# Kernel tuning notes

Hardware: AMD Instinct MI355X
Metric: run time of the kernel (lower is better)

Reference implementation:

```python
import jax, jax.numpy as jnp
import numpy as np

IN_DIM, OUT_DIM, N_PROTO, RANK = 1024, 1024, 32, 16


def setup_inputs() -> dict:
    key = jax.random.key(0)
    ks = jax.random.split(key, 5)
    x = jax.random.normal(ks[0], (2, 4096, IN_DIM), dtype=jnp.float32)
    prototypes = jax.random.normal(ks[1], (N_PROTO, IN_DIM), dtype=jnp.float32) * 0.02
    B = jax.random.normal(ks[2], (N_PROTO, RANK, IN_DIM), dtype=jnp.float32) * 0.02
    A = jax.random.normal(ks[3], (N_PROTO, OUT_DIM, RANK), dtype=jnp.float32) * 0.02
    bias = jnp.zeros((N_PROTO, OUT_DIM), dtype=jnp.float32)
    temp = jnp.asarray(1.0, dtype=jnp.float32)
    return {"x": x, "prototypes": prototypes, "B": B, "A": A, "bias": bias, "temp": temp}


def reference(x, prototypes, B, A, bias, temp):
    lead = x.shape[:-1]
    xf = x.reshape(-1, IN_DIM)                       # [N, in]
    x2 = jnp.sum(xf * xf, axis=1, keepdims=True)     # [N,1]
    p2 = jnp.sum(prototypes * prototypes, axis=1)    # [P]
    d2 = x2 + p2[None, :] - 2.0 * (xf @ prototypes.T)
    dists = jnp.sqrt(jnp.maximum(d2, 0.0))           # [N,P]
    t = jnp.maximum(jnp.abs(temp), 0.1)
    w = jax.nn.softmax(-dists / t, axis=1)           # [N,P]
    topw, topi = jax.lax.top_k(w, 2)                 # [N,2]
    topw = topw / jnp.sum(topw, axis=1, keepdims=True)
    out = jnp.zeros((xf.shape[0], OUT_DIM), dtype=xf.dtype)
    for tslot in range(2):
        idx = topi[:, tslot]                          # [N]
        wt = topw[:, tslot:tslot + 1]                 # [N,1]
        h = jnp.einsum('nri,ni->nr', B[idx], xf)      # gathered low-rank down-proj
        y = jnp.einsum('nor,nr->no', A[idx], h) + bias[idx]
        out = out + wt * y
    return out.reshape(*lead, OUT_DIM)
```

## Files before the change

kernel.cpp:

```cpp
#include <hip/hip_runtime.h>
#include <math.h>

#define ROWS_TOTAL 8192
#define KDIM 1024
#define NPROTO 32
#define RNK 16
#define OUTD 1024
#define TIE_EPS 1.30e-4

__global__ __launch_bounds__(256) void route_kernel(
    const float* __restrict__ x, const float* __restrict__ proto,
    const float* __restrict__ temp, float4* __restrict__ route,
    int* __restrict__ counts)
{
    __shared__ float Xs[16][68];
    __shared__ float Ps[64][33];
    __shared__ double x2s[16];
    __shared__ double p2s[32];
    __shared__ int lcnt[64];

    const int tid = threadIdx.x;
    const int rowbase = blockIdx.x * 16;
    const int frow = tid >> 4;
    const int fq   = tid & 15;
    const int c    = tid & 31;
    const int rg   = tid >> 5;

    if (tid < 64) lcnt[tid] = 0;

    double xsq = 0.0, p2a = 0.0, p2b = 0.0;
    double acc0 = 0.0, acc1 = 0.0;

    for (int kc = 0; kc < KDIM; kc += 64) {
        float4 xv = *(const float4*)(x + (rowbase + frow) * KDIM + kc + 4 * fq);
        xsq = fma((double)xv.x, (double)xv.x, xsq);
        xsq = fma((double)xv.y, (double)xv.y, xsq);
        xsq = fma((double)xv.z, (double)xv.z, xsq);
        xsq = fma((double)xv.w, (double)xv.w, xsq);
        *(float4*)(&Xs[frow][4 * fq]) = xv;
        float4 pa = *(const float4*)(proto + frow * KDIM + kc + 4 * fq);
        float4 pb = *(const float4*)(proto + (frow + 16) * KDIM + kc + 4 * fq);
        p2a = fma((double)pa.x, (double)pa.x, p2a);
        p2a = fma((double)pa.y, (double)pa.y, p2a);
        p2a = fma((double)pa.z, (double)pa.z, p2a);
        p2a = fma((double)pa.w, (double)pa.w, p2a);
        p2b = fma((double)pb.x, (double)pb.x, p2b);
        p2b = fma((double)pb.y, (double)pb.y, p2b);
        p2b = fma((double)pb.z, (double)pb.z, p2b);
        p2b = fma((double)pb.w, (double)pb.w, p2b);
        Ps[4 * fq + 0][frow] = pa.x;
        Ps[4 * fq + 1][frow] = pa.y;
        Ps[4 * fq + 2][frow] = pa.z;
        Ps[4 * fq + 3][frow] = pa.w;
        Ps[4 * fq + 0][frow + 16] = pb.x;
        Ps[4 * fq + 1][frow + 16] = pb.y;
        Ps[4 * fq + 2][frow + 16] = pb.z;
        Ps[4 * fq + 3][frow + 16] = pb.w;
        __syncthreads();
        #pragma unroll
        for (int k = 0; k < 64; k += 4) {
            float4 xa = *(const float4*)(&Xs[2 * rg][k]);
            float4 xb = *(const float4*)(&Xs[2 * rg + 1][k]);
            double q0 = (double)Ps[k][c],     q1 = (double)Ps[k + 1][c];
            double q2 = (double)Ps[k + 2][c], q3 = (double)Ps[k + 3][c];
            acc0 = fma((double)xa.x, q0, acc0);
            acc0 = fma((double)xa.y, q1, acc0);
            acc0 = fma((double)xa.z, q2, acc0);
            acc0 = fma((double)xa.w, q3, acc0);
            acc1 = fma((double)xb.x, q0, acc1);
            acc1 = fma((double)xb.y, q1, acc1);
            acc1 = fma((double)xb.z, q2, acc1);
            acc1 = fma((double)xb.w, q3, acc1);
        }
        __syncthreads();
    }

    #pragma unroll
    for (int m = 1; m < 16; m <<= 1) {
        xsq += __shfl_xor(xsq, m);
        p2a += __shfl_xor(p2a, m);
        p2b += __shfl_xor(p2b, m);
    }
    if (fq == 0) { x2s[frow] = xsq; p2s[frow] = p2a; p2s[frow + 16] = p2b; }
    __syncthreads();

    const double tmp = (double)fmaxf(fabsf(temp[0]), 0.1f);
    const double myp2 = p2s[c];

    #pragma unroll
    for (int which = 0; which < 2; ++which) {
        double key = myp2 - 2.0 * (which ? acc1 : acc0);
        double k1 = key, k2 = 1.0e300, k3 = 1.1e300;
        int    i1 = c,   i2 = 64,      i3 = 65;
        #pragma unroll
        for (int m = 1; m < 32; m <<= 1) {
            double b1 = __shfl_xor(k1, m), b2 = __shfl_xor(k2, m), b3 = __shfl_xor(k3, m);
            int    j1 = __shfl_xor(i1, m), j2 = __shfl_xor(i2, m), j3 = __shfl_xor(i3, m);
            bool c1 = k1 <= b1;
            double m1 = c1 ? k1 : b1, M1 = c1 ? b1 : k1;
            int   mi1 = c1 ? i1 : j1, Mi1 = c1 ? j1 : i1;
            bool c2 = k2 <= b2;
            double m2 = c2 ? k2 : b2;
            int   mi2 = c2 ? i2 : j2;
            bool c3 = k3 <= b3;
            double m3 = c3 ? k3 : b3;
            int   mi3 = c3 ? i3 : j3;
            bool c4 = M1 <= m2;
            double t2 = c4 ? M1 : m2,  T2 = c4 ? m2 : M1;
            int   ti2 = c4 ? Mi1 : mi2, Ti2 = c4 ? mi2 : Mi1;
            bool c5 = T2 <= m3;
            k1 = m1; i1 = mi1;
            k2 = t2; i2 = ti2;
            k3 = c5 ? T2 : m3; i3 = c5 ? Ti2 : mi3;
        }
        if (c == 0) {
            const int row = rowbase + 2 * rg + which;
            bool tie = (k3 - k2) < TIE_EPS;
            bool take3 = tie && (i3 < i2);
            double ksel = take3 ? k3 : k2;
            int    isel = take3 ? i3 : i2;
            double x2 = x2s[2 * rg + which];
            double d0 = sqrt(fmax(x2 + k1, 0.0));
            double d1 = sqrt(fmax(x2 + ksel, 0.0));
            float e  = expf((float)((d0 - d1) / tmp));
            float w0 = 1.f / (1.f + e);
            route[row] = make_float4(__int_as_float(i1), __int_as_float(isel),
                                     w0, e * w0);
            atomicAdd(&lcnt[i1], 1);
            atomicAdd(&lcnt[32 + isel], 1);
        }
    }
    __syncthreads();
    if (tid < 64) atomicAdd(&counts[tid], lcnt[tid]);
}

__global__ __launch_bounds__(64) void scan_kernel(int* __restrict__ counts,
                                                  int2* __restrict__ segs)
{
    const int tid = threadIdx.x;
    int v = counts[tid];
    int sum = v;
    #pragma unroll
    for (int off = 1; off < 32; off <<= 1) {
        int u = __shfl_up(sum, off, 32);
        if ((tid & 31) >= off) sum += u;
    }
    int excl = sum - v;
    counts[tid] = excl;
    segs[tid] = make_int2(excl, excl + v);
}

__global__ __launch_bounds__(256) void scatter_kernel(
    const float4* __restrict__ route, int* __restrict__ counts,
    int* __restrict__ rowlist0, int* __restrict__ rowlist1)
{
    __shared__ int lcnt[64];
    __shared__ int gbase[64];
    const int tid = threadIdx.x;
    const int i = blockIdx.x * 256 + tid;
    if (tid < 64) lcnt[tid] = 0;
    __syncthreads();
    float4 rt = route[i];
    int p0 = __float_as_int(rt.x);
    int p1 = __float_as_int(rt.y);
    int lp0 = atomicAdd(&lcnt[p0], 1);
    int lp1 = atomicAdd(&lcnt[32 + p1], 1);
    __syncthreads();
    if (tid < 64) gbase[tid] = atomicAdd(&counts[tid], lcnt[tid]);
    __syncthreads();
    rowlist0[gbase[p0] + lp0] = i;
    rowlist1[gbase[32 + p1] + lp1] = i;
}

__global__ __launch_bounds__(256) void transpose_kernel(
    const float* __restrict__ A, const float* __restrict__ B,
    float* __restrict__ At, float* __restrict__ Bt)
{
    __shared__ float T[16 * 68];
    __shared__ float U[64 * 20];
    const int tid = threadIdx.x;
    const int p = blockIdx.x;
    const float4* B4 = (const float4*)(B + (size_t)p * RNK * KDIM);
    const float4* A4 = (const float4*)(A + (size_t)p * OUTD * RNK);
    float4* Bt4 = (float4*)(Bt + (size_t)p * KDIM * RNK);
    float4* At4 = (float4*)(At + (size_t)p * RNK * OUTD);

    for (int c = 0; c < 16; ++c) {
        {
            int r = tid >> 4, kk = tid & 15;
            float4 v = B4[r * 256 + c * 16 + kk];
            *(float4*)&T[r * 68 + kk * 4] = v;
        }
        {
            int o = tid >> 2, rq = tid & 3;
            float4 v = A4[(c * 64 + o) * 4 + rq];
            *(float4*)&U[o * 20 + rq * 4] = v;
        }
        __syncthreads();
        {
            int k = tid >> 2, rq = tid & 3;
            float4 g = make_float4(T[(rq * 4 + 0) * 68 + k], T[(rq * 4 + 1) * 68 + k],
                                   T[(rq * 4 + 2) * 68 + k], T[(rq * 4 + 3) * 68 + k]);
            Bt4[(c * 64 + k) * 4 + rq] = g;
        }
        {
            int r = tid >> 4, ow = tid & 15;
            float4 g = make_float4(U[(ow * 4 + 0) * 20 + r], U[(ow * 4 + 1) * 20 + r],
                                   U[(ow * 4 + 2) * 20 + r], U[(ow * 4 + 3) * 20 + r]);
            At4[r * 256 + c * 16 + ow] = g;
        }
        __syncthreads();
    }
}

__global__ __launch_bounds__(256) void h_kernel(
    const float* __restrict__ x, const float* __restrict__ Bt,
    const int* __restrict__ rowlist0, const int* __restrict__ rowlist1,
    const int2* __restrict__ segs, float* __restrict__ hws)
{
    __shared__ float part[4][4][17];
    __shared__ int xoffs[4];

    const int tid = threadIdx.x;
    const int w = tid >> 6, l = tid & 63;
    const int kq = l >> 2, rq = l & 3;
    const int s = blockIdx.y;
    const int slot = s >> 5;
    const int2 sg = segs[s];
    const int* rl = slot ? rowlist1 : rowlist0;
    const float4* Btp = (const float4*)(Bt + (size_t)(s & 31) * KDIM * RNK);
    const int qbase = w * 256;

    for (int c = blockIdx.x; ; c += gridDim.x) {
        const int base = sg.x + c * 4;
        if (base >= sg.y) break;
        const int m = min(4, sg.y - base);

        if (tid < 4) xoffs[tid] = rl[base + min(tid, m - 1)] * KDIM;
        __syncthreads();
        const int x0 = xoffs[0], x1 = xoffs[1], x2 = xoffs[2], x3 = xoffs[3];

        float4 a0 = {0,0,0,0}, a1 = {0,0,0,0}, a2 = {0,0,0,0}, a3 = {0,0,0,0};
        #pragma unroll
        for (int i = 0; i < 16; ++i) {
            const int k = qbase + i * 16 + kq;
            float4 bv = Btp[k * 4 + rq];
            float v0 = x[x0 + k], v1 = x[x1 + k], v2 = x[x2 + k], v3 = x[x3 + k];
            a0.x = fmaf(v0, bv.x, a0.x); a0.y = fmaf(v0, bv.y, a0.y);
            a0.z = fmaf(v0, bv.z, a0.z); a0.w = fmaf(v0, bv.w, a0.w);
            a1.x = fmaf(v1, bv.x, a1.x); a1.y = fmaf(v1, bv.y, a1.y);
            a1.z = fmaf(v1, bv.z, a1.z); a1.w = fmaf(v1, bv.w, a1.w);
            a2.x = fmaf(v2, bv.x, a2.x); a2.y = fmaf(v2, bv.y, a2.y);
            a2.z = fmaf(v2, bv.z, a2.z); a2.w = fmaf(v2, bv.w, a2.w);
            a3.x = fmaf(v3, bv.x, a3.x); a3.y = fmaf(v3, bv.y, a3.y);
            a3.z = fmaf(v3, bv.z, a3.z); a3.w = fmaf(v3, bv.w, a3.w);
        }
        #pragma unroll
        for (int msk = 4; msk < 64; msk <<= 1) {
            a0.x += __shfl_xor(a0.x, msk); a0.y += __shfl_xor(a0.y, msk);
            a0.z += __shfl_xor(a0.z, msk); a0.w += __shfl_xor(a0.w, msk);
            a1.x += __shfl_xor(a1.x, msk); a1.y += __shfl_xor(a1.y, msk);
            a1.z += __shfl_xor(a1.z, msk); a1.w += __shfl_xor(a1.w, msk);
            a2.x += __shfl_xor(a2.x, msk); a2.y += __shfl_xor(a2.y, msk);
            a2.z += __shfl_xor(a2.z, msk); a2.w += __shfl_xor(a2.w, msk);
            a3.x += __shfl_xor(a3.x, msk); a3.y += __shfl_xor(a3.y, msk);
            a3.z += __shfl_xor(a3.z, msk); a3.w += __shfl_xor(a3.w, msk);
        }
        if (kq == 0) {
            *(float4*)&part[w][0][rq * 4] = a0;
            *(float4*)&part[w][1][rq * 4] = a1;
            *(float4*)&part[w][2][rq * 4] = a2;
            *(float4*)&part[w][3][rq * 4] = a3;
        }
        __syncthreads();
        if (tid < 64) {
            const int e = tid >> 4, r = tid & 15;
            if (e < m) {
                float hsum = part[0][e][r] + part[1][e][r]
                           + part[2][e][r] + part[3][e][r];
                hws[(size_t)(slot * ROWS_TOTAL + base + e) * 16 + r] = hsum;
            }
        }
        __syncthreads();
    }
}

__global__ __launch_bounds__(64) void y_kernel(
    const float* __restrict__ At, const float* __restrict__ bias,
    const float4* __restrict__ route, const int* __restrict__ rowlist,
    const int2* __restrict__ segs, const float* __restrict__ hws,
    float* __restrict__ out, int slot)
{
    __shared__ float hsm[4][16];
    __shared__ int rows[4];
    __shared__ float wts[4];

    const int l = threadIdx.x;
    const int p = blockIdx.y;
    const int2 sg = segs[slot * 32 + p];
    const float4* Atp = (const float4*)(At + (size_t)p * RNK * OUTD);
    const float4* bp  = (const float4*)(bias + (size_t)p * OUTD);

    for (int c = blockIdx.x; ; c += gridDim.x) {
        const int base = sg.x + c * 4;
        if (base >= sg.y) break;
        const int m = min(4, sg.y - base);
        const int gbase = slot * ROWS_TOTAL + base;

        if (l < 4) {
            int rr = rowlist[base + min(l, m - 1)];
            rows[l] = rr;
            float4 rt = route[rr];
            wts[l] = slot ? rt.w : rt.z;
        }
        {
            const int e = l >> 4, r = l & 15;
            hsm[e][r] = hws[(size_t)(gbase + min(e, m - 1)) * 16 + r];
        }
        __syncthreads();

        #pragma unroll
        for (int j = 0; j < 4; ++j) {
            const int f4 = j * 64 + l;
            float4 bb = bp[f4];
            float4 c0 = bb, c1 = bb, c2 = bb, c3 = bb;
            #pragma unroll
            for (int r = 0; r < 16; ++r) {
                float4 a = Atp[r * 256 + f4];
                float h0 = hsm[0][r], h1 = hsm[1][r], h2 = hsm[2][r], h3 = hsm[3][r];
                c0.x = fmaf(h0, a.x, c0.x); c0.y = fmaf(h0, a.y, c0.y);
                c0.z = fmaf(h0, a.z, c0.z); c0.w = fmaf(h0, a.w, c0.w);
                c1.x = fmaf(h1, a.x, c1.x); c1.y = fmaf(h1, a.y, c1.y);
                c1.z = fmaf(h1, a.z, c1.z); c1.w = fmaf(h1, a.w, c1.w);
                c2.x = fmaf(h2, a.x, c2.x); c2.y = fmaf(h2, a.y, c2.y);
                c2.z = fmaf(h2, a.z, c2.z); c2.w = fmaf(h2, a.w, c2.w);
                c3.x = fmaf(h3, a.x, c3.x); c3.y = fmaf(h3, a.y, c3.y);
                c3.z = fmaf(h3, a.z, c3.z); c3.w = fmaf(h3, a.w, c3.w);
            }
            #pragma unroll
            for (int e = 0; e < 4; ++e) {
                if (e < m) {
                    float4 cc = (e == 0) ? c0 : (e == 1) ? c1 : (e == 2) ? c2 : c3;
                    const float w = wts[e];
                    float4 v = make_float4(w * cc.x, w * cc.y, w * cc.z, w * cc.w);
                    float4* dst = (float4*)(out + (size_t)rows[e] * OUTD + f4 * 4);
                    if (slot) {
                        float4 old = *dst;
                        v.x += old.x; v.y += old.y; v.z += old.z; v.w += old.w;
                    }
                    *dst = v;
                }
            }
        }
        __syncthreads();
    }
}

extern "C" void kernel_launch(void* const* d_in, const int* in_sizes, int n_in,
                              void* d_out, int out_size, void* d_ws, size_t ws_size,
                              hipStream_t stream) {
    const float* x     = (const float*)d_in[0];
    const float* proto = (const float*)d_in[1];
    const float* B     = (const float*)d_in[2];
    const float* A     = (const float*)d_in[3];
    const float* bias  = (const float*)d_in[4];
    const float* temp  = (const float*)d_in[5];
    float* out = (float*)d_out;

    char* wsb = (char*)d_ws;
    float4* route = (float4*)wsb;
    int* rowlist0 = (int*)(wsb + 131072);
    int* rowlist1 = rowlist0 + ROWS_TOTAL;
    int* counts   = rowlist1 + ROWS_TOTAL;
    int2* segs    = (int2*)(counts + 64);
    float* Bt     = (float*)(wsb + 262144);
    float* At     = (float*)(wsb + 262144 + 2097152);
    float* hws    = (float*)(wsb + 262144 + 2 * 2097152);

    hipMemsetAsync(counts, 0, 64 * sizeof(int), stream);
    transpose_kernel<<<NPROTO, 256, 0, stream>>>(A, B, At, Bt);
    route_kernel<<<ROWS_TOTAL / 16, 256, 0, stream>>>(x, proto, temp, route, counts);
    scan_kernel<<<1, 64, 0, stream>>>(counts, segs);
    scatter_kernel<<<ROWS_TOTAL / 256, 256, 0, stream>>>(route, counts, rowlist0, rowlist1);
    h_kernel<<<dim3(64, 64), 256, 0, stream>>>(x, Bt, rowlist0, rowlist1, segs, hws);
    y_kernel<<<dim3(64, NPROTO), 64, 0, stream>>>(At, bias, route, rowlist0, segs, hws, out, 0);
    y_kernel<<<dim3(64, NPROTO), 64, 0, stream>>>(At, bias, route, rowlist1, segs, hws, out, 1);
}
```

Before: 175.4 us.

## Restructure routing distance kernel with 4x4 register tiles and split-K reduction

The routing kernel now processes 8 rows per block instead of 16 and stages x and prototypes in shared memory as doubles. Each thread computes a 4x4 register tile over a K slice, followed by shuffle and shared-memory reductions across K lanes and warps. Prototype squared norms move into a separate one-block kernel, so blocks no longer recompute them, and the row norm is accumulated in fp32. This aims to cut per-FMA shared loads and conversions and to double the block count, at the cost of more shared memory, an extra launch, and slightly different rounding of x² near ties.

```diff
diff --git a/kernel.cpp b/kernel.cpp
--- a/kernel.cpp
+++ b/kernel.cpp
@@ -8,127 +8,171 @@
 #define OUTD 1024
 #define TIE_EPS 1.30e-4
 
+__global__ __launch_bounds__(256) void p2_kernel(
+    const float* __restrict__ proto, double* __restrict__ p2g)
+{
+    __shared__ double red[32][9];
+    const int t = threadIdx.x;
+    const int p = t >> 3, seg = t & 7;
+    const float* a = proto + (size_t)p * KDIM + seg * 128;
+    double s = 0.0;
+    for (int k = 0; k < 128; ++k) {
+        double v = (double)a[k];
+        s = fma(v, v, s);
+    }
+    red[p][seg] = s;
+    __syncthreads();
+    if (t < 32) {
+        double acc = red[t][0];
+        #pragma unroll
+        for (int j = 1; j < 8; ++j) acc += red[t][j];
+        p2g[t] = acc;
+    }
+}
+
 __global__ __launch_bounds__(256) void route_kernel(
     const float* __restrict__ x, const float* __restrict__ proto,
-    const float* __restrict__ temp, float4* __restrict__ route,
-    int* __restrict__ counts)
-{
-    __shared__ float Xs[16][68];
-    __shared__ float Ps[64][33];
-    __shared__ double x2s[16];
-    __shared__ double p2s[32];
+    const float* __restrict__ temp, const double* __restrict__ p2g,
+    float4* __restrict__ route, int* __restrict__ counts)
+{
+    __shared__ double Xs64[8][65];
+    __shared__ double Ps64[32][65];
+    __shared__ double part[4][8][33];
+    __shared__ float x2s[8];
     __shared__ int lcnt[64];
 
     const int tid = threadIdx.x;
-    const int rowbase = blockIdx.x * 16;
-    const int frow = tid >> 4;
-    const int fq   = tid & 15;
-    const int c    = tid & 31;
-    const int rg   = tid >> 5;
+    const int l = tid & 63;
+    const int w = tid >> 6;
+    const int kslane = l & 3;
+    const int cq = (l >> 2) & 7;
+    const int rq = l >> 5;
+    const int rowbase = blockIdx.x * 8;
 
     if (tid < 64) lcnt[tid] = 0;
 
-    double xsq = 0.0, p2a = 0.0, p2b = 0.0;
-    double acc0 = 0.0, acc1 = 0.0;
+    const int sfrow = tid >> 4 & 15;
+    const int sfq   = tid & 15;
+
+    float xsq = 0.f;
+    double a00=0,a01=0,a02=0,a03=0, a10=0,a11=0,a12=0,a13=0;
+    double a20=0,a21=0,a22=0,a23=0, a30=0,a31=0,a32=0,a33=0;
 
     for (int kc = 0; kc < KDIM; kc += 64) {
-        float4 xv = *(const float4*)(x + (rowbase + frow) * KDIM + kc + 4 * fq);
-        xsq = fma((double)xv.x, (double)xv.x, xsq);
-        xsq = fma((double)xv.y, (double)xv.y, xsq);
-        xsq = fma((double)xv.z, (double)xv.z, xsq);
-        xsq = fma((double)xv.w, (double)xv.w, xsq);
-        *(float4*)(&Xs[frow][4 * fq]) = xv;
-        float4 pa = *(const float4*)(proto + frow * KDIM + kc + 4 * fq);
-        float4 pb = *(const float4*)(proto + (frow + 16) * KDIM + kc + 4 * fq);
-        p2a = fma((double)pa.x, (double)pa.x, p2a);
-        p2a = fma((double)pa.y, (double)pa.y, p2a);
-        p2a = fma((double)pa.z, (double)pa.z, p2a);
-        p2a = fma((double)pa.w, (double)pa.w, p2a);
-        p2b = fma((double)pb.x, (double)pb.x, p2b);
-        p2b = fma((double)pb.y, (double)pb.y, p2b);
-        p2b = fma((double)pb.z, (double)pb.z, p2b);
-        p2b = fma((double)pb.w, (double)pb.w, p2b);
-        Ps[4 * fq + 0][frow] = pa.x;
-        Ps[4 * fq + 1][frow] = pa.y;
-        Ps[4 * fq + 2][frow] = pa.z;
-        Ps[4 * fq + 3][frow] = pa.w;
-        Ps[4 * fq + 0][frow + 16] = pb.x;
-        Ps[4 * fq + 1][frow + 16] = pb.y;
-        Ps[4 * fq + 2][frow + 16] = pb.z;
-        Ps[4 * fq + 3][frow + 16] = pb.w;
-        __syncthreads();
+        if (tid < 128) {
+            float4 xv = *(const float4*)(x + (size_t)(rowbase + (tid >> 4)) * KDIM + kc + 4 * sfq);
+            xsq = fmaf(xv.x, xv.x, fmaf(xv.y, xv.y, fmaf(xv.z, xv.z, fmaf(xv.w, xv.w, xsq))));
+            double* d = &Xs64[tid >> 4][4 * sfq];
+            d[0] = (double)xv.x; d[1] = (double)xv.y;
+            d[2] = (double)xv.z; d[3] = (double)xv.w;
+        }
+        {
+            float4 pa = *(const float4*)(proto + (size_t)sfrow * KDIM + kc + 4 * sfq);
+            float4 pb = *(const float4*)(proto + (size_t)(sfrow + 16) * KDIM + kc + 4 * sfq);
+            double* da = &Ps64[sfrow][4 * sfq];
+            double* db = &Ps64[sfrow + 16][4 * sfq];
+            da[0] = (double)pa.x; da[1] = (double)pa.y;
+            da[2] = (double)pa.z; da[3] = (double)pa.w;
+            db[0] = (double)pb.x; db[1] = (double)pb.y;
+            db[2] = (double)pb.z; db[3] = (double)pb.w;
+        }
+        __syncthreads();
+
+        const int kb = w * 16 + kslane * 4;
         #pragma unroll
-        for (int k = 0; k < 64; k += 4) {
-            float4 xa = *(const float4*)(&Xs[2 * rg][k]);
-            float4 xb = *(const float4*)(&Xs[2 * rg + 1][k]);
-            double q0 = (double)Ps[k][c],     q1 = (double)Ps[k + 1][c];
-            double q2 = (double)Ps[k + 2][c], q3 = (double)Ps[k + 3][c];
-            acc0 = fma((double)xa.x, q0, acc0);
-            acc0 = fma((double)xa.y, q1, acc0);
-            acc0 = fma((double)xa.z, q2, acc0);
-            acc0 = fma((double)xa.w, q3, acc0);
-            acc1 = fma((double)xb.x, q0, acc1);
-            acc1 = fma((double)xb.y, q1, acc1);
-            acc1 = fma((double)xb.z, q2, acc1);
-            acc1 = fma((double)xb.w, q3, acc1);
+        for (int j = 0; j < 4; ++j) {
+            const int k = kb + j;
+            double x0 = Xs64[4 * rq + 0][k];
+            double x1 = Xs64[4 * rq + 1][k];
+            double x2 = Xs64[4 * rq + 2][k];
+            double x3 = Xs64[4 * rq + 3][k];
+            double q0 = Ps64[cq][k];
+            double q1 = Ps64[cq + 8][k];
+            double q2 = Ps64[cq + 16][k];
+            double q3 = Ps64[cq + 24][k];
+            a00 = fma(x0, q0, a00); a01 = fma(x0, q1, a01);
+            a02 = fma(x0, q2, a02); a03 = fma(x0, q3, a03);
+            a10 = fma(x1, q0, a10); a11 = fma(x1, q1, a11);
+            a12 = fma(x1, q2, a12); a13 = fma(x1, q3, a13);
+            a20 = fma(x2, q0, a20); a21 = fma(x2, q1, a21);
+            a22 = fma(x2, q2, a22); a23 = fma(x2, q3, a23);
+            a30 = fma(x3, q0, a30); a31 = fma(x3, q1, a31);
+            a32 = fma(x3, q2, a32); a33 = fma(x3, q3, a33);
         }
         __syncthreads();
     }
 
     #pragma unroll
-    for (int m = 1; m < 16; m <<= 1) {
-        xsq += __shfl_xor(xsq, m);
-        p2a += __shfl_xor(p2a, m);
-        p2b += __shfl_xor(p2b, m);
-    }
-    if (fq == 0) { x2s[frow] = xsq; p2s[frow] = p2a; p2s[frow + 16] = p2b; }
-    __syncthreads();
-
-    const double tmp = (double)fmaxf(fabsf(temp[0]), 0.1f);
-    const double myp2 = p2s[c];
-
+    for (int m = 1; m < 4; m <<= 1) {
+        a00 += __shfl_xor(a00, m); a01 += __shfl_xor(a01, m);
+        a02 += __shfl_xor(a02, m); a03 += __shfl_xor(a03, m);
+        a10 += __shfl_xor(a10, m); a11 += __shfl_xor(a11, m);
+        a12 += __shfl_xor(a12, m); a13 += __shfl_xor(a13, m);
+        a20 += __shfl_xor(a20, m); a21 += __shfl_xor(a21, m);
+        a22 += __shfl_xor(a22, m); a23 += __shfl_xor(a23, m);
+        a30 += __shfl_xor(a30, m); a31 += __shfl_xor(a31, m);
+        a32 += __shfl_xor(a32, m); a33 += __shfl_xor(a33, m);
+    }
+    if (kslane == 0) {
+        part[w][4 * rq + 0][cq] = a00; part[w][4 * rq + 0][cq + 8]  = a01;
+        part[w][4 * rq + 0][cq + 16] = a02; part[w][4 * rq + 0][cq + 24] = a03;
+        part[w][4 * rq + 1][cq] = a10; part[w][4 * rq + 1][cq + 8]  = a11;
+        part[w][4 * rq + 1][cq + 16] = a12; part[w][4 * rq + 1][cq + 24] = a13;
+        part[w][4 * rq + 2][cq] = a20; part[w][4 * rq + 2][cq + 8]  = a21;
+        part[w][4 * rq + 2][cq + 16] = a22; part[w][4 * rq + 2][cq + 24] = a23;
+        part[w][4 * rq + 3][cq] = a30; part[w][4 * rq + 3][cq + 8]  = a31;
+        part[w][4 * rq + 3][cq + 16] = a32; part[w][4 * rq + 3][cq + 24] = a33;
+    }
     #pragma unroll
-    for (int which = 0; which < 2; ++which) {
-        double key = myp2 - 2.0 * (which ? acc1 : acc0);
-        double k1 = key, k2 = 1.0e300, k3 = 1.1e300;
-        int    i1 = c,   i2 = 64,      i3 = 65;
-        #pragma unroll
-        for (int m = 1; m < 32; m <<= 1) {
-            double b1 = __shfl_xor(k1, m), b2 = __shfl_xor(k2, m), b3 = __shfl_xor(k3, m);
-            int    j1 = __shfl_xor(i1, m), j2 = __shfl_xor(i2, m), j3 = __shfl_xor(i3, m);
-            bool c1 = k1 <= b1;
-            double m1 = c1 ? k1 : b1, M1 = c1 ? b1 : k1;
-            int   mi1 = c1 ? i1 : j1, Mi1 = c1 ? j1 : i1;
-            bool c2 = k2 <= b2;
-            double m2 = c2 ? k2 : b2;
-            int   mi2 = c2 ? i2 : j2;
-            bool c3 = k3 <= b3;
-            double m3 = c3 ? k3 : b3;
-            int   mi3 = c3 ? i3 : j3;
-            bool c4 = M1 <= m2;
-            double t2 = c4 ? M1 : m2,  T2 = c4 ? m2 : M1;
-            int   ti2 = c4 ? Mi1 : mi2, Ti2 = c4 ? mi2 : Mi1;
-            bool c5 = T2 <= m3;
-            k1 = m1; i1 = mi1;
-            k2 = t2; i2 = ti2;
-            k3 = c5 ? T2 : m3; i3 = c5 ? Ti2 : mi3;
-        }
-        if (c == 0) {
-            const int row = rowbase + 2 * rg + which;
-            bool tie = (k3 - k2) < TIE_EPS;
-            bool take3 = tie && (i3 < i2);
-            double ksel = take3 ? k3 : k2;
-            int    isel = take3 ? i3 : i2;
-            double x2 = x2s[2 * rg + which];
-            double d0 = sqrt(fmax(x2 + k1, 0.0));
-            double d1 = sqrt(fmax(x2 + ksel, 0.0));
-            float e  = expf((float)((d0 - d1) / tmp));
-            float w0 = 1.f / (1.f + e);
-            route[row] = make_float4(__int_as_float(i1), __int_as_float(isel),
-                                     w0, e * w0);
-            atomicAdd(&lcnt[i1], 1);
-            atomicAdd(&lcnt[32 + isel], 1);
-        }
+    for (int m = 1; m < 16; m <<= 1) xsq += __shfl_xor(xsq, m);
+    if (tid < 128 && sfq == 0) x2s[tid >> 4] = xsq;
+    __syncthreads();
+
+    const int selrow = 2 * w + rq;
+    const int c = l & 31;
+    double dsum = ((part[0][selrow][c] + part[1][selrow][c])
+                 + part[2][selrow][c]) + part[3][selrow][c];
+    double key = p2g[c] - 2.0 * dsum;
+
+    double k1 = key, k2 = 1.0e300, k3 = 1.1e300;
+    int    i1 = c,   i2 = 64,      i3 = 65;
+    #pragma unroll
+    for (int m = 1; m < 32; m <<= 1) {
+        double b1 = __shfl_xor(k1, m), b2 = __shfl_xor(k2, m), b3 = __shfl_xor(k3, m);
+        int    j1 = __shfl_xor(i1, m), j2 = __shfl_xor(i2, m), j3 = __shfl_xor(i3, m);
+        bool c1 = k1 <= b1;
+        double m1 = c1 ? k1 : b1, M1 = c1 ? b1 : k1;
+        int   mi1 = c1 ? i1 : j1, Mi1 = c1 ? j1 : i1;
+        bool c2 = k2 <= b2;
+        double m2 = c2 ? k2 : b2;
+        int   mi2 = c2 ? i2 : j2;
+        bool c3 = k3 <= b3;
+        double m3 = c3 ? k3 : b3;
+        int   mi3 = c3 ? i3 : j3;
+        bool c4 = M1 <= m2;
+        double t2 = c4 ? M1 : m2,  T2 = c4 ? m2 : M1;
+        int   ti2 = c4 ? Mi1 : mi2, Ti2 = c4 ? mi2 : Mi1;
+        bool c5 = T2 <= m3;
+        k1 = m1; i1 = mi1;
+        k2 = t2; i2 = ti2;
+        k3 = c5 ? T2 : m3; i3 = c5 ? Ti2 : mi3;
+    }
+    if (c == 0) {
+        const double tmp = (double)fmaxf(fabsf(temp[0]), 0.1f);
+        const int row = rowbase + selrow;
+        bool tie = (k3 - k2) < TIE_EPS;
+        bool take3 = tie && (i3 < i2);
+        double ksel = take3 ? k3 : k2;
+        int    isel = take3 ? i3 : i2;
+        double x2 = (double)x2s[selrow];
+        double d0 = sqrt(fmax(x2 + k1, 0.0));
+        double d1 = sqrt(fmax(x2 + ksel, 0.0));
+        float e  = expf((float)((d0 - d1) / tmp));
+        float w0 = 1.f / (1.f + e);
+        route[row] = make_float4(__int_as_float(i1), __int_as_float(isel),
+                                 w0, e * w0);
+        atomicAdd(&lcnt[i1], 1);
+        atomicAdd(&lcnt[32 + isel], 1);
     }
     __syncthreads();
     if (tid < 64) atomicAdd(&counts[tid], lcnt[tid]);
@@ -373,13 +417,15 @@
     int* rowlist1 = rowlist0 + ROWS_TOTAL;
     int* counts   = rowlist1 + ROWS_TOTAL;
     int2* segs    = (int2*)(counts + 64);
+    double* p2g   = (double*)(wsb + 197376);
     float* Bt     = (float*)(wsb + 262144);
     float* At     = (float*)(wsb + 262144 + 2097152);
     float* hws    = (float*)(wsb + 262144 + 2 * 2097152);
 
     hipMemsetAsync(counts, 0, 64 * sizeof(int), stream);
+    p2_kernel<<<1, 256, 0, stream>>>(proto, p2g);
     transpose_kernel<<<NPROTO, 256, 0, stream>>>(A, B, At, Bt);
-    route_kernel<<<ROWS_TOTAL / 16, 256, 0, stream>>>(x, proto, temp, route, counts);
+    route_kernel<<<ROWS_TOTAL / 8, 256, 0, stream>>>(x, proto, temp, p2g, route, counts);
     scan_kernel<<<1, 64, 0, stream>>>(counts, segs);
     scatter_kernel<<<ROWS_TOTAL / 256, 256, 0, stream>>>(route, counts, rowlist0, rowlist1);
     h_kernel<<<dim3(64, 64), 256, 0, stream>>>(x, Bt, rowlist0, rowlist1, segs, hws);
```

Result: slower. 181.0 us (+3.2%).

## Route in fp32 with a double-precision refine pass for ambiguous rows

Applied to the files above, without the earlier changes.

The routing kernel now computes distances and top-k in fp32 rather than fp64. It uses a pre-transposed prototype matrix built in a merged prep kernel that also computes prototype norms once. Rows whose top-4 keys are close enough to make the selection ambiguous are flagged and recomputed in double precision by a single-block refine kernel, which also performs the count scan. This removes the heavy fp64 FMA cost of routing, but adds a serial refine pass whose cost grows with the number of flagged rows, which is capped at a fixed size.

```diff
diff --git a/kernel.cpp b/kernel.cpp
--- a/kernel.cpp
+++ b/kernel.cpp
@@ -7,147 +7,309 @@
 #define RNK 16
 #define OUTD 1024
 #define TIE_EPS 1.30e-4
+#define DELTA 4.0e-5f
+#define FLAG_CAP 4096
+
+__global__ __launch_bounds__(256) void prep_kernel(
+    const float* __restrict__ A, const float* __restrict__ B,
+    const float* __restrict__ proto, float* __restrict__ At,
+    float* __restrict__ Bt, float* __restrict__ Pt, double* __restrict__ p2g)
+{
+    __shared__ float T[16 * 68];
+    __shared__ float U[64 * 20];
+    __shared__ double red[32][9];
+    __shared__ float TP[32][33];
+    const int tid = threadIdx.x;
+
+    if (blockIdx.x < 32) {
+        const int p = blockIdx.x;
+        const float4* B4 = (const float4*)(B + (size_t)p * RNK * KDIM);
+        const float4* A4 = (const float4*)(A + (size_t)p * OUTD * RNK);
+        float4* Bt4 = (float4*)(Bt + (size_t)p * KDIM * RNK);
+        float4* At4 = (float4*)(At + (size_t)p * RNK * OUTD);
+        for (int c = 0; c < 16; ++c) {
+            {
+                int r = tid >> 4, kk = tid & 15;
+                float4 v = B4[r * 256 + c * 16 + kk];
+                *(float4*)&T[r * 68 + kk * 4] = v;
+            }
+            {
+                int o = tid >> 2, rq = tid & 3;
+                float4 v = A4[(c * 64 + o) * 4 + rq];
+                *(float4*)&U[o * 20 + rq * 4] = v;
+            }
+            __syncthreads();
+            {
+                int k = tid >> 2, rq = tid & 3;
+                float4 g = make_float4(T[(rq * 4 + 0) * 68 + k], T[(rq * 4 + 1) * 68 + k],
+                                       T[(rq * 4 + 2) * 68 + k], T[(rq * 4 + 3) * 68 + k]);
+                Bt4[(c * 64 + k) * 4 + rq] = g;
+            }
+            {
+                int r = tid >> 4, ow = tid & 15;
+                float4 g = make_float4(U[(ow * 4 + 0) * 20 + r], U[(ow * 4 + 1) * 20 + r],
+                                       U[(ow * 4 + 2) * 20 + r], U[(ow * 4 + 3) * 20 + r]);
+                At4[r * 256 + c * 16 + ow] = g;
+            }
+            __syncthreads();
+        }
+    } else {
+        {
+            const int p = tid >> 3, seg = tid & 7;
+            const float* a = proto + (size_t)p * KDIM + seg * 128;
+            double s = 0.0;
+            for (int k = 0; k < 128; ++k) {
+                double v = (double)a[k];
+                s = fma(v, v, s);
+            }
+            red[p][seg] = s;
+        }
+        __syncthreads();
+        if (tid < 32) {
+            double acc = red[tid][0];
+            #pragma unroll
+            for (int j = 1; j < 8; ++j) acc += red[tid][j];
+            p2g[tid] = acc;
+        }
+        float4* Pt4 = (float4*)Pt;
+        for (int kc = 0; kc < 32; ++kc) {
+            {
+                int cc = tid >> 3, kk4 = tid & 7;
+                float4 v = *(const float4*)(proto + (size_t)cc * KDIM + kc * 32 + kk4 * 4);
+                TP[cc][kk4 * 4 + 0] = v.x; TP[cc][kk4 * 4 + 1] = v.y;
+                TP[cc][kk4 * 4 + 2] = v.z; TP[cc][kk4 * 4 + 3] = v.w;
+            }
+            __syncthreads();
+            {
+                int kk = tid >> 3, c4 = tid & 7;
+                float4 g = make_float4(TP[c4 * 4 + 0][kk], TP[c4 * 4 + 1][kk],
+                                       TP[c4 * 4 + 2][kk], TP[c4 * 4 + 3][kk]);
+                Pt4[(kc * 32 + kk) * 8 + c4] = g;
+            }
+            __syncthreads();
+        }
+    }
+}
+
+#define INS(kb, ib) { \
+    bool lt1 = (kb) < k1, lt2 = (kb) < k2, lt3 = (kb) < k3, lt4 = (kb) < k4; \
+    float nk4 = lt3 ? k3 : (lt4 ? (kb) : k4); int ni4 = lt3 ? i3 : (lt4 ? (ib) : i4); \
+    float nk3 = lt2 ? k2 : (lt3 ? (kb) : k3); int ni3 = lt2 ? i2 : (lt3 ? (ib) : i3); \
+    float nk2 = lt1 ? k1 : (lt2 ? (kb) : k2); int ni2 = lt1 ? i1 : (lt2 ? (ib) : i2); \
+    k4 = nk4; i4 = ni4; k3 = nk3; i3 = ni3; k2 = nk2; i2 = ni2; \
+    if (lt1) { k1 = (kb); i1 = (ib); } }
 
 __global__ __launch_bounds__(256) void route_kernel(
-    const float* __restrict__ x, const float* __restrict__ proto,
-    const float* __restrict__ temp, float4* __restrict__ route,
-    int* __restrict__ counts)
+    const float* __restrict__ x, const float* __restrict__ Pt,
+    const float* __restrict__ temp, const double* __restrict__ p2g,
+    float4* __restrict__ route, int* __restrict__ counts,
+    int* __restrict__ flagcnt, int* __restrict__ flaglist)
 {
-    __shared__ float Xs[16][68];
-    __shared__ float Ps[64][33];
-    __shared__ double x2s[16];
-    __shared__ double p2s[32];
+    __shared__ float Xs[8 * KDIM];
+    __shared__ float part[4][8][33];
+    __shared__ float x2p[4][8];
     __shared__ int lcnt[64];
 
     const int tid = threadIdx.x;
-    const int rowbase = blockIdx.x * 16;
-    const int frow = tid >> 4;
-    const int fq   = tid & 15;
-    const int c    = tid & 31;
-    const int rg   = tid >> 5;
+    const int w = tid >> 6, l = tid & 63;
+    const int c4 = l & 7, kslot = l >> 3;
+    const int rowbase = blockIdx.x * 8;
 
     if (tid < 64) lcnt[tid] = 0;
 
-    double xsq = 0.0, p2a = 0.0, p2b = 0.0;
-    double acc0 = 0.0, acc1 = 0.0;
-
-    for (int kc = 0; kc < KDIM; kc += 64) {
-        float4 xv = *(const float4*)(x + (rowbase + frow) * KDIM + kc + 4 * fq);
-        xsq = fma((double)xv.x, (double)xv.x, xsq);
-        xsq = fma((double)xv.y, (double)xv.y, xsq);
-        xsq = fma((double)xv.z, (double)xv.z, xsq);
-        xsq = fma((double)xv.w, (double)xv.w, xsq);
-        *(float4*)(&Xs[frow][4 * fq]) = xv;
-        float4 pa = *(const float4*)(proto + frow * KDIM + kc + 4 * fq);
-        float4 pb = *(const float4*)(proto + (frow + 16) * KDIM + kc + 4 * fq);
-        p2a = fma((double)pa.x, (double)pa.x, p2a);
-        p2a = fma((double)pa.y, (double)pa.y, p2a);
-        p2a = fma((double)pa.z, (double)pa.z, p2a);
-        p2a = fma((double)pa.w, (double)pa.w, p2a);
-        p2b = fma((double)pb.x, (double)pb.x, p2b);
-        p2b = fma((double)pb.y, (double)pb.y, p2b);
-        p2b = fma((double)pb.z, (double)pb.z, p2b);
-        p2b = fma((double)pb.w, (double)pb.w, p2b);
-        Ps[4 * fq + 0][frow] = pa.x;
-        Ps[4 * fq + 1][frow] = pa.y;
-        Ps[4 * fq + 2][frow] = pa.z;
-        Ps[4 * fq + 3][frow] = pa.w;
-        Ps[4 * fq + 0][frow + 16] = pb.x;
-        Ps[4 * fq + 1][frow + 16] = pb.y;
-        Ps[4 * fq + 2][frow + 16] = pb.z;
-        Ps[4 * fq + 3][frow + 16] = pb.w;
-        __syncthreads();
-        #pragma unroll
-        for (int k = 0; k < 64; k += 4) {
-            float4 xa = *(const float4*)(&Xs[2 * rg][k]);
-            float4 xb = *(const float4*)(&Xs[2 * rg + 1][k]);
-            double q0 = (double)Ps[k][c],     q1 = (double)Ps[k + 1][c];
-            double q2 = (double)Ps[k + 2][c], q3 = (double)Ps[k + 3][c];
-            acc0 = fma((double)xa.x, q0, acc0);
-            acc0 = fma((double)xa.y, q1, acc0);
-            acc0 = fma((double)xa.z, q2, acc0);
-            acc0 = fma((double)xa.w, q3, acc0);
-            acc1 = fma((double)xb.x, q0, acc1);
-            acc1 = fma((double)xb.y, q1, acc1);
-            acc1 = fma((double)xb.z, q2, acc1);
-            acc1 = fma((double)xb.w, q3, acc1);
-        }
-        __syncthreads();
-    }
-
+    const float4* x4 = (const float4*)x;
+    float sq[8];
     #pragma unroll
-    for (int m = 1; m < 16; m <<= 1) {
-        xsq += __shfl_xor(xsq, m);
-        p2a += __shfl_xor(p2a, m);
-        p2b += __shfl_xor(p2b, m);
-    }
-    if (fq == 0) { x2s[frow] = xsq; p2s[frow] = p2a; p2s[frow + 16] = p2b; }
-    __syncthreads();
-
-    const double tmp = (double)fmaxf(fabsf(temp[0]), 0.1f);
-    const double myp2 = p2s[c];
-
+    for (int j = 0; j < 8; ++j) {
+        float4 v = x4[(size_t)rowbase * 256 + j * 256 + tid];
+        ((float4*)Xs)[j * 256 + tid] = v;
+        sq[j] = fmaf(v.x, v.x, fmaf(v.y, v.y, fmaf(v.z, v.z, v.w * v.w)));
+    }
     #pragma unroll
-    for (int which = 0; which < 2; ++which) {
-        double key = myp2 - 2.0 * (which ? acc1 : acc0);
-        double k1 = key, k2 = 1.0e300, k3 = 1.1e300;
-        int    i1 = c,   i2 = 64,      i3 = 65;
+    for (int m = 1; m < 64; m <<= 1) {
+        #pragma unroll
+        for (int j = 0; j < 8; ++j) sq[j] += __shfl_xor(sq[j], m);
+    }
+    if (l == 0) {
+        #pragma unroll
+        for (int j = 0; j < 8; ++j) x2p[w][j] = sq[j];
+    }
+    __syncthreads();
+
+    float acc[8][4];
+    #pragma unroll
+    for (int j = 0; j < 8; ++j)
+        #pragma unroll
+        for (int jj = 0; jj < 4; ++jj) acc[j][jj] = 0.f;
+
+    const float4* Pt4 = (const float4*)Pt;
+    const int kbase = w * 256;
+    #pragma unroll 4
+    for (int i = 0; i < 32; ++i) {
+        const int k = kbase + i * 8 + kslot;
+        float4 pv = Pt4[k * 8 + c4];
+        #pragma unroll
+        for (int j = 0; j < 8; ++j) {
+            float xv = Xs[j * KDIM + k];
+            acc[j][0] = fmaf(xv, pv.x, acc[j][0]);
+            acc[j][1] = fmaf(xv, pv.y, acc[j][1]);
+            acc[j][2] = fmaf(xv, pv.z, acc[j][2]);
+            acc[j][3] = fmaf(xv, pv.w, acc[j][3]);
+        }
+    }
+    #pragma unroll
+    for (int m = 8; m < 64; m <<= 1) {
+        #pragma unroll
+        for (int j = 0; j < 8; ++j) {
+            acc[j][0] += __shfl_xor(acc[j][0], m);
+            acc[j][1] += __shfl_xor(acc[j][1], m);
+            acc[j][2] += __shfl_xor(acc[j][2], m);
+            acc[j][3] += __shfl_xor(acc[j][3], m);
+        }
+    }
+    if (kslot == 0) {
+        #pragma unroll
+        for (int j = 0; j < 8; ++j) {
+            part[w][j][4 * c4 + 0] = acc[j][0];
+            part[w][j][4 * c4 + 1] = acc[j][1];
+            part[w][j][4 * c4 + 2] = acc[j][2];
+            part[w][j][4 * c4 + 3] = acc[j][3];
+        }
+    }
+    __syncthreads();
+
+    {
+        const int rowsel = tid >> 5, c = tid & 31;
+        float dsum = (part[0][rowsel][c] + part[1][rowsel][c])
+                   + (part[2][rowsel][c] + part[3][rowsel][c]);
+        float key = (float)(p2g[c] - 2.0 * (double)dsum);
+        float x2 = (x2p[0][rowsel] + x2p[1][rowsel])
+                 + (x2p[2][rowsel] + x2p[3][rowsel]);
+
+        float k1 = key, k2 = 3.0e38f, k3 = 3.1e38f, k4 = 3.2e38f;
+        int i1 = c, i2 = 64, i3 = 65, i4 = 66;
         #pragma unroll
         for (int m = 1; m < 32; m <<= 1) {
-            double b1 = __shfl_xor(k1, m), b2 = __shfl_xor(k2, m), b3 = __shfl_xor(k3, m);
-            int    j1 = __shfl_xor(i1, m), j2 = __shfl_xor(i2, m), j3 = __shfl_xor(i3, m);
-            bool c1 = k1 <= b1;
-            double m1 = c1 ? k1 : b1, M1 = c1 ? b1 : k1;
-            int   mi1 = c1 ? i1 : j1, Mi1 = c1 ? j1 : i1;
-            bool c2 = k2 <= b2;
-            double m2 = c2 ? k2 : b2;
-            int   mi2 = c2 ? i2 : j2;
-            bool c3 = k3 <= b3;
-            double m3 = c3 ? k3 : b3;
-            int   mi3 = c3 ? i3 : j3;
-            bool c4 = M1 <= m2;
-            double t2 = c4 ? M1 : m2,  T2 = c4 ? m2 : M1;
-            int   ti2 = c4 ? Mi1 : mi2, Ti2 = c4 ? mi2 : Mi1;
-            bool c5 = T2 <= m3;
-            k1 = m1; i1 = mi1;
-            k2 = t2; i2 = ti2;
-            k3 = c5 ? T2 : m3; i3 = c5 ? Ti2 : mi3;
+            float b1 = __shfl_xor(k1, m), b2 = __shfl_xor(k2, m);
+            float b3 = __shfl_xor(k3, m), b4 = __shfl_xor(k4, m);
+            int j1 = __shfl_xor(i1, m), j2 = __shfl_xor(i2, m);
+            int j3 = __shfl_xor(i3, m), j4 = __shfl_xor(i4, m);
+            INS(b1, j1); INS(b2, j2); INS(b3, j3); INS(b4, j4);
         }
         if (c == 0) {
-            const int row = rowbase + 2 * rg + which;
-            bool tie = (k3 - k2) < TIE_EPS;
+            const int row = rowbase + rowsel;
+            const float tf = fmaxf(fabsf(temp[0]), 0.1f);
+            bool amb = (k2 - k1 < DELTA) || (k3 - k2 < DELTA)
+                    || (fabsf((k3 - k2) - (float)TIE_EPS) < DELTA)
+                    || (k4 - k3 < DELTA);
+            bool tie = (k3 - k2) < (float)TIE_EPS;
             bool take3 = tie && (i3 < i2);
-            double ksel = take3 ? k3 : k2;
-            int    isel = take3 ? i3 : i2;
-            double x2 = x2s[2 * rg + which];
-            double d0 = sqrt(fmax(x2 + k1, 0.0));
-            double d1 = sqrt(fmax(x2 + ksel, 0.0));
-            float e  = expf((float)((d0 - d1) / tmp));
+            float ksel = take3 ? k3 : k2;
+            int   isel = take3 ? i3 : i2;
+            float d0 = sqrtf(fmaxf(x2 + k1, 0.f));
+            float d1 = sqrtf(fmaxf(x2 + ksel, 0.f));
+            float e = expf((d0 - d1) / tf);
             float w0 = 1.f / (1.f + e);
             route[row] = make_float4(__int_as_float(i1), __int_as_float(isel),
                                      w0, e * w0);
             atomicAdd(&lcnt[i1], 1);
             atomicAdd(&lcnt[32 + isel], 1);
+            if (amb) {
+                int fi = atomicAdd(flagcnt, 1);
+                if (fi < FLAG_CAP) flaglist[fi] = row;
+            }
         }
     }
     __syncthreads();
     if (tid < 64) atomicAdd(&counts[tid], lcnt[tid]);
 }
 
-__global__ __launch_bounds__(64) void scan_kernel(int* __restrict__ counts,
-                                                  int2* __restrict__ segs)
+__global__ __launch_bounds__(256) void refine_scan_kernel(
+    const float* __restrict__ x, const float* __restrict__ proto,
+    const float* __restrict__ temp, const double* __restrict__ p2g,
+    float4* __restrict__ route, int* __restrict__ counts,
+    const int* __restrict__ flagcnt, const int* __restrict__ flaglist,
+    int2* __restrict__ segs)
 {
     const int tid = threadIdx.x;
-    int v = counts[tid];
-    int sum = v;
-    #pragma unroll
-    for (int off = 1; off < 32; off <<= 1) {
-        int u = __shfl_up(sum, off, 32);
-        if ((tid & 31) >= off) sum += u;
-    }
-    int excl = sum - v;
-    counts[tid] = excl;
-    segs[tid] = make_int2(excl, excl + v);
+    const int w = tid >> 6, l = tid & 63;
+    const int c = l & 31, half = l >> 5;
+    const int n = min(flagcnt[0], FLAG_CAP);
+
+    for (int f = w; f < n; f += 4) {
+        const int row = flaglist[f];
+        const float* xr = x + (size_t)row * KDIM;
+        double xs = 0.0;
+        for (int k = l * 16; k < l * 16 + 16; ++k) {
+            double v = (double)xr[k];
+            xs = fma(v, v, xs);
+        }
+        #pragma unroll
+        for (int m = 1; m < 64; m <<= 1) xs += __shfl_xor(xs, m);
+        const float* pr = proto + (size_t)c * KDIM + half * 512;
+        const float* xh = xr + half * 512;
+        double d0a = 0.0, d1a = 0.0;
+        for (int k = 0; k < 512; k += 2) {
+            d0a = fma((double)xh[k], (double)pr[k], d0a);
+            d1a = fma((double)xh[k + 1], (double)pr[k + 1], d1a);
+        }
+        double acc = d0a + d1a;
+        acc += __shfl_xor(acc, 32);
+        double key = p2g[c] - 2.0 * acc;
+
+        double k1 = key, k2 = 1.0e300, k3 = 1.1e300;
+        int i1 = c, i2 = 64, i3 = 65;
+        #pragma unroll
+        for (int m = 1; m < 32; m <<= 1) {
+            double b1 = __shfl_xor(k1, m), b2 = __shfl_xor(k2, m), b3 = __shfl_xor(k3, m);
+            int j1 = __shfl_xor(i1, m), j2 = __shfl_xor(i2, m), j3 = __shfl_xor(i3, m);
+            bool c1 = (k1 < b1) || (k1 == b1 && i1 < j1);
+            double m1 = c1 ? k1 : b1, M1 = c1 ? b1 : k1;
+            int mi1 = c1 ? i1 : j1, Mi1 = c1 ? j1 : i1;
+            bool c2 = (k2 < b2) || (k2 == b2 && i2 < j2);
+            double m2 = c2 ? k2 : b2;
+            int mi2 = c2 ? i2 : j2;
+            bool c3 = (k3 < b3) || (k3 == b3 && i3 < j3);
+            double m3 = c3 ? k3 : b3;
+            int mi3 = c3 ? i3 : j3;
+            bool c4 = (M1 < m2) || (M1 == m2 && Mi1 < mi2);
+            double t2 = c4 ? M1 : m2, T2 = c4 ? m2 : M1;
+            int ti2 = c4 ? Mi1 : mi2, Ti2 = c4 ? mi2 : Mi1;
+            bool c5 = (T2 < m3) || (T2 == m3 && Ti2 < mi3);
+            k1 = m1; i1 = mi1;
+            k2 = t2; i2 = ti2;
+            k3 = c5 ? T2 : m3; i3 = c5 ? Ti2 : mi3;
+        }
+        if (l == 0) {
+            const double tmp = (double)fmaxf(fabsf(temp[0]), 0.1f);
+            bool tie = (k3 - k2) < TIE_EPS;
+            bool take3 = tie && (i3 < i2);
+            double ksel = take3 ? k3 : k2;
+            int isel = take3 ? i3 : i2;
+            double dd0 = sqrt(fmax(xs + k1, 0.0));
+            double dd1 = sqrt(fmax(xs + ksel, 0.0));
+            float e = expf((float)((dd0 - dd1) / tmp));
+            float w0 = 1.f / (1.f + e);
+            float4 old = route[row];
+            int oi1 = __float_as_int(old.x), oisel = __float_as_int(old.y);
+            if (oi1 != i1) { atomicAdd(&counts[oi1], -1); atomicAdd(&counts[i1], 1); }
+            if (oisel != isel) { atomicAdd(&counts[32 + oisel], -1); atomicAdd(&counts[32 + isel], 1); }
+            route[row] = make_float4(__int_as_float(i1), __int_as_float(isel),
+                                     w0, e * w0);
+        }
+    }
+    __syncthreads();
+    if (tid < 64) {
+        int v = atomicAdd(&counts[tid], 0);
+        int sum = v;
+        #pragma unroll
+        for (int off = 1; off < 32; off <<= 1) {
+            int u = __shfl_up(sum, off, 32);
+            if ((tid & 31) >= off) sum += u;
+        }
+        counts[tid] = sum - v;
+        segs[tid] = make_int2(sum - v, sum);
+    }
 }
 
 __global__ __launch_bounds__(256) void scatter_kernel(
@@ -170,47 +332,6 @@
     __syncthreads();
     rowlist0[gbase[p0] + lp0] = i;
     rowlist1[gbase[32 + p1] + lp1] = i;
-}
-
-__global__ __launch_bounds__(256) void transpose_kernel(
-    const float* __restrict__ A, const float* __restrict__ B,
-    float* __restrict__ At, float* __restrict__ Bt)
-{
-    __shared__ float T[16 * 68];
-    __shared__ float U[64 * 20];
-    const int tid = threadIdx.x;
-    const int p = blockIdx.x;
-    const float4* B4 = (const float4*)(B + (size_t)p * RNK * KDIM);
-    const float4* A4 = (const float4*)(A + (size_t)p * OUTD * RNK);
-    float4* Bt4 = (float4*)(Bt + (size_t)p * KDIM * RNK);
-    float4* At4 = (float4*)(At + (size_t)p * RNK * OUTD);
-
-    for (int c = 0; c < 16; ++c) {
-        {
-            int r = tid >> 4, kk = tid & 15;
-            float4 v = B4[r * 256 + c * 16 + kk];
-            *(float4*)&T[r * 68 + kk * 4] = v;
-        }
-        {
-            int o = tid >> 2, rq = tid & 3;
-            float4 v = A4[(c * 64 + o) * 4 + rq];
-            *(float4*)&U[o * 20 + rq * 4] = v;
-        }
-        __syncthreads();
-        {
-            int k = tid >> 2, rq = tid & 3;
-            float4 g = make_float4(T[(rq * 4 + 0) * 68 + k], T[(rq * 4 + 1) * 68 + k],
-                                   T[(rq * 4 + 2) * 68 + k], T[(rq * 4 + 3) * 68 + k]);
-            Bt4[(c * 64 + k) * 4 + rq] = g;
-        }
-        {
-            int r = tid >> 4, ow = tid & 15;
-            float4 g = make_float4(U[(ow * 4 + 0) * 20 + r], U[(ow * 4 + 1) * 20 + r],
-                                   U[(ow * 4 + 2) * 20 + r], U[(ow * 4 + 3) * 20 + r]);
-            At4[r * 256 + c * 16 + ow] = g;
-        }
-        __syncthreads();
-    }
 }
 
 __global__ __launch_bounds__(256) void h_kernel(
@@ -371,16 +492,22 @@
     float4* route = (float4*)wsb;
     int* rowlist0 = (int*)(wsb + 131072);
     int* rowlist1 = rowlist0 + ROWS_TOTAL;
-    int* counts   = rowlist1 + ROWS_TOTAL;
-    int2* segs    = (int2*)(counts + 64);
-    float* Bt     = (float*)(wsb + 262144);
-    float* At     = (float*)(wsb + 262144 + 2097152);
-    float* hws    = (float*)(wsb + 262144 + 2 * 2097152);
-
-    hipMemsetAsync(counts, 0, 64 * sizeof(int), stream);
-    transpose_kernel<<<NPROTO, 256, 0, stream>>>(A, B, At, Bt);
-    route_kernel<<<ROWS_TOTAL / 16, 256, 0, stream>>>(x, proto, temp, route, counts);
-    scan_kernel<<<1, 64, 0, stream>>>(counts, segs);
+    int* counts   = (int*)(wsb + 196608);
+    int2* segs    = (int2*)(wsb + 196864);
+    double* p2g   = (double*)(wsb + 197376);
+    int* flagcnt  = (int*)(wsb + 197632);
+    int* flaglist = (int*)(wsb + 197760);
+    float* Pt     = (float*)(wsb + 262144);
+    float* Bt     = (float*)(wsb + 393216);
+    float* At     = (float*)(wsb + 393216 + 2097152);
+    float* hws    = (float*)(wsb + 393216 + 2 * 2097152);
+
+    hipMemsetAsync(wsb + 196608, 0, 1156, stream);
+    prep_kernel<<<33, 256, 0, stream>>>(A, B, proto, At, Bt, Pt, p2g);
+    route_kernel<<<ROWS_TOTAL / 8, 256, 0, stream>>>(x, Pt, temp, p2g, route,
+                                                     counts, flagcnt, flaglist);
+    refine_scan_kernel<<<1, 256, 0, stream>>>(x, proto, temp, p2g, route,
+                                              counts, flagcnt, flaglist, segs);
     scatter_kernel<<<ROWS_TOTAL / 256, 256, 0, stream>>>(route, counts, rowlist0, rowlist1);
     h_kernel<<<dim3(64, 64), 256, 0, stream>>>(x, Bt, rowlist0, rowlist1, segs, hws);
     y_kernel<<<dim3(64, NPROTO), 64, 0, stream>>>(At, bias, route, rowlist0, segs, hws, out, 0);
```

After: 195.5 us. 1.11x slower.
